# Optimization experiments

Measured on AMD Instinct MI355X. Metric: run time of the kernel, lower is better.

The kernel has to match this reference:

```python
import jax, jax.numpy as jnp
import numpy as np

B, N, D = 4, 4096, 1024
LN_EPS = 1e-5

def setup_inputs() -> dict:
    key = jax.random.key(0)
    ks = jax.random.split(key, 12)
    s = 1.0 / np.sqrt(D)
    return {
        "embeddings": jax.random.normal(ks[0], (B, N, D), dtype=jnp.float32),
        "edge_indices": jax.random.randint(ks[1], (2, 8192), 0, N, dtype=jnp.int64),
        "edge_times": jax.random.uniform(ks[2], (8192,), dtype=jnp.float32),
        "timestamps": jax.random.uniform(ks[3], (N,), dtype=jnp.float32),
        "Wq": jax.random.uniform(ks[4], (D, D), jnp.float32, -s, s),
        "bq": jax.random.uniform(ks[5], (D,), jnp.float32, -s, s),
        "Wk": jax.random.uniform(ks[6], (D, D), jnp.float32, -s, s),
        "bk": jax.random.uniform(ks[7], (D,), jnp.float32, -s, s),
        "Wv": jax.random.uniform(ks[8], (D, D), jnp.float32, -s, s),
        "bv": jax.random.uniform(ks[9], (D,), jnp.float32, -s, s),
        "gamma": jnp.ones((D,), jnp.float32),
        "beta": jnp.zeros((D,), jnp.float32),
    }

def reference(embeddings, edge_indices, edge_times, timestamps,
              Wq, bq, Wk, bk, Wv, bv, gamma, beta):
    # edge_indices / edge_times / timestamps are unused by the original forward.
    d = embeddings.shape[-1]
    q = jnp.einsum("bnd,ed->bne", embeddings, Wq) + bq   # [B,N,D]
    k = jnp.einsum("bnd,ed->bne", embeddings, Wk) + bk
    v = jnp.einsum("bnd,ed->bne", embeddings, Wv) + bv
    scores = jnp.einsum("bnd,bmd->bnm", q, k) / jnp.sqrt(jnp.asarray(d, embeddings.dtype))
    attn = jax.nn.softmax(scores, axis=-1)                # [B,N,N]
    attended = jnp.einsum("bnm,bmd->bnd", attn, v)
    x = embeddings + attended
    mu = jnp.mean(x, axis=-1, keepdims=True)
    var = jnp.mean(jnp.square(x - mu), axis=-1, keepdims=True)
    return gamma * (x - mu) * jax.lax.rsqrt(var + LN_EPS) + beta
```

## Files before the change

kernel.cpp:

```cpp
#include <hip/hip_runtime.h>
#include <hip/hip_fp8.h>

typedef unsigned short u16;
typedef unsigned char  u8;
typedef long long      i64;
using bf16x8 = __attribute__((ext_vector_type(8))) __bf16;
using f32x4  = __attribute__((ext_vector_type(4))) float;
using i64x2  = __attribute__((ext_vector_type(2))) long long;

__device__ __forceinline__ u16 f2bf(float f) {
    unsigned u = __builtin_bit_cast(unsigned, f);
    u += 0x7fffu + ((u >> 16) & 1u);
    return (u16)(u >> 16);
}
__device__ __forceinline__ float bf2f(u16 h) {
    unsigned u = ((unsigned)h) << 16;
    return __builtin_bit_cast(float, u);
}
__device__ __forceinline__ u8 f2fp8(float f) {
    __hip_fp8_e4m3 t(f);
    return t.__x;
}
__device__ __forceinline__ float wred_sum(float v) {
    #pragma unroll
    for (int o = 32; o; o >>= 1) v += __shfl_xor(v, o, 64);
    return v;
}

__device__ __forceinline__ void gl2lds16(const void* g, void* l) {
    __builtin_amdgcn_global_load_lds(
        (__attribute__((address_space(1))) void*)(g),
        (__attribute__((address_space(3))) void*)(l), 16, 0, 0);
}

#define SBAR0() __builtin_amdgcn_sched_barrier(0)

__global__ __launch_bounds__(256)
void cast_bf16(const float* __restrict__ src, u16* __restrict__ dst, int n4) {
    int i = blockIdx.x * 256 + threadIdx.x;
    if (i < n4) {
        float4 f = ((const float4*)src)[i];
        ushort4 u;
        u.x = f2bf(f.x); u.y = f2bf(f.y); u.z = f2bf(f.z); u.w = f2bf(f.w);
        ((ushort4*)dst)[i] = u;
    }
}

template<int MODE>
__global__ __launch_bounds__(512, 2)
void gemm256(const u16* __restrict__ A, const u16* __restrict__ Bt,
             u16* __restrict__ oQ, u16* __restrict__ oK,
             const float* __restrict__ bQ, const float* __restrict__ bK,
             const float* __restrict__ bV,
             u8* __restrict__ oP, u8* __restrict__ oP2,
             float* __restrict__ sums, const float scale)
{
    __shared__ u16 smem[65536];
    const int tid = threadIdx.x;
    const int wv = tid >> 6, lane = tid & 63;
    const int wm = wv >> 2, wn = wv & 3;
    const int row0 = blockIdx.x << 8, col0 = blockIdx.y << 8;

    const size_t boff = (size_t)blockIdx.z * 4194304;
    const int srow = tid >> 2;
    const int scol = ((tid & 3) ^ ((tid >> 3) & 3)) << 3;
    const u16* gA = A + boff + (size_t)(row0 + srow) * 1024 + scol;
    const u16* gB = Bt + boff + (size_t)(col0 + srow) * 1024 + scol;
    char* lds = (char*)smem;
    const int wvo = wv << 10;

    const int fr = lane & 15, g = lane >> 4;
    const int kc = (g ^ ((fr >> 1) & 3)) << 4;

    f32x4 acc[8][4];
    #pragma unroll
    for (int i = 0; i < 8; i++)
        #pragma unroll
        for (int j = 0; j < 4; j++) acc[i][j] = (f32x4){0.f, 0.f, 0.f, 0.f};

    #define SG_A(ts, sl) { \
        gl2lds16(gA + (ts) * 32,          lds + (sl) * 32768 + wvo); \
        gl2lds16(gA + 131072 + (ts) * 32, lds + (sl) * 32768 + 8192 + wvo); }
    #define SG_B(ts, sl) { \
        gl2lds16(gB + (ts) * 32,          lds + (sl) * 32768 + 16384 + wvo); \
        gl2lds16(gB + 131072 + (ts) * 32, lds + (sl) * 32768 + 24576 + wvo); }

    SG_A(0, 0); SG_B(0, 0);
    SG_A(1, 1); SG_B(1, 1);
    SG_A(2, 2); SG_B(2, 2);
    asm volatile("s_waitcnt vmcnt(8)" ::: "memory");
    __builtin_amdgcn_s_barrier();
    SBAR0();

    for (int t = 0; t < 32; ++t) {
        const int slot = t & 3;
        const int ts = (t + 3) & 31;
        const int ns = (t + 3) & 3;
        const char* Ab = lds + slot * 32768;
        const char* Bb = Ab + 16384;

        SG_A(ts, ns);
        bf16x8 bf[4], af[4];
        #pragma unroll
        for (int j = 0; j < 4; ++j)
            bf[j] = *(const bf16x8*)(Bb + (wn * 64 + 16 * j + fr) * 64 + kc);
        #pragma unroll
        for (int i = 0; i < 4; ++i)
            af[i] = *(const bf16x8*)(Ab + (wm * 128 + 16 * i + fr) * 64 + kc);
        SBAR0();
        __builtin_amdgcn_s_barrier();
        asm volatile("s_waitcnt lgkmcnt(0)" ::: "memory");
        SBAR0();
        __builtin_amdgcn_s_setprio(1);
        #pragma unroll
        for (int i = 0; i < 4; ++i)
            #pragma unroll
            for (int j = 0; j < 4; ++j)
                acc[i][j] = __builtin_amdgcn_mfma_f32_16x16x32_bf16(af[i], bf[j], acc[i][j], 0, 0, 0);
        __builtin_amdgcn_s_setprio(0);

        SG_B(ts, ns);
        bf16x8 af2[4];
        #pragma unroll
        for (int i = 0; i < 4; ++i)
            af2[i] = *(const bf16x8*)(Ab + (wm * 128 + 64 + 16 * i + fr) * 64 + kc);
        asm volatile("s_waitcnt vmcnt(8) lgkmcnt(0)" ::: "memory");
        SBAR0();
        __builtin_amdgcn_s_barrier();
        SBAR0();
        __builtin_amdgcn_s_setprio(1);
        #pragma unroll
        for (int i = 0; i < 4; ++i)
            #pragma unroll
            for (int j = 0; j < 4; ++j)
                acc[i + 4][j] = __builtin_amdgcn_mfma_f32_16x16x32_bf16(af2[i], bf[j], acc[i + 4][j], 0, 0, 0);
        __builtin_amdgcn_s_setprio(0);
    }
    #undef SG_A
    #undef SG_B

    asm volatile("s_waitcnt vmcnt(0)" ::: "memory");

    const int rB = (lane >> 4) << 2, cB = lane & 15;

    if (MODE == 0) {
        const int sel = col0 >> 10;
        if (sel < 2) {
            const float* bias = (sel == 0) ? bQ : bK;
            u16* dst = (sel == 0) ? oQ : oK;
            #pragma unroll
            for (int i = 0; i < 8; i++) {
                #pragma unroll
                for (int j = 0; j < 4; j++) {
                    const int m0 = row0 + wm * 128 + 16 * i + rB;
                    const int e  = (col0 & 1023) + wn * 64 + 16 * j + cB;
                    const float bb = bias[e];
                    #pragma unroll
                    for (int t = 0; t < 4; t++)
                        dst[(size_t)(m0 + t) * 1024 + e] = f2bf(acc[i][j][t] + bb);
                }
            }
        } else {
            const int b      = row0 >> 12;
            const int n_base = row0 & 4095;
            const int e0     = col0 & 1023;
            unsigned* lds32 = (unsigned*)smem;
            __syncthreads();
            #pragma unroll
            for (int i = 0; i < 8; i++) {
                const int n_l0 = wm * 128 + 16 * i + rB;
                const int blk  = n_l0 >> 6;
                const int q    = (n_l0 & 63) >> 2;
                const int pd   = ((q >> 1) & 3) * 4 + ((q >> 3) << 1) + (q & 1);
                const int dwi  = blk * 16 + pd;
                const int G    = dwi >> 2;
                const int kq   = dwi & 3;
                #pragma unroll
                for (int j = 0; j < 4; j++) {
                    const int e_p = wn * 64 + 16 * j + cB;
                    const float bb = bV[e0 + e_p];
                    union { u8 c[4]; unsigned u; } pk;
                    pk.c[0] = f2fp8(acc[i][j][0] + bb);
                    pk.c[1] = f2fp8(acc[i][j][1] + bb);
                    pk.c[2] = f2fp8(acc[i][j][2] + bb);
                    pk.c[3] = f2fp8(acc[i][j][3] + bb);
                    lds32[e_p * 64 + ((G ^ (e_p & 15)) << 2) + kq] = pk.u;
                }
            }
            __syncthreads();
            #pragma unroll
            for (int it = 0; it < 8; ++it) {
                const int idx = it * 512 + tid;
                const int er  = idx >> 4;
                const int c16 = idx & 15;
                int4 v = *(const int4*)&lds32[er * 64 + ((c16 ^ (er & 15)) << 2)];
                *(int4*)&oP[(size_t)b * 4194304 +
                            (size_t)(e0 + er) * 4096 + n_base + c16 * 16] = v;
            }
        }
    } else {
        u8* Pz = blockIdx.z ? oP2 : oP;
        float* smz = sums + (blockIdx.z << 12);
        float psum[8][4];
        #pragma unroll
        for (int i = 0; i < 8; i++)
            #pragma unroll
            for (int t = 0; t < 4; t++) psum[i][t] = 0.f;

        #pragma unroll
        for (int i = 0; i < 8; i++) {
            const int m0 = row0 + wm * 128 + 16 * i + rB;
            #pragma unroll
            for (int j = 0; j < 4; j++) {
                const int n64 = 16 * j + cB;
                const int p   = ((n64 >> 3) & 3) * 16 + ((n64 >> 5) << 3) + (cB & 7);
                const int c   = col0 + wn * 64 + p;
                #pragma unroll
                for (int t = 0; t < 4; t++) {
                    const float e = __expf(acc[i][j][t] * scale);
                    psum[i][t] += e;
                    Pz[(size_t)(m0 + t) * 4096 + c] = f2fp8(e);
                }
            }
        }
        #pragma unroll
        for (int i = 0; i < 8; i++) {
            #pragma unroll
            for (int t = 0; t < 4; t++) {
                float v = psum[i][t];
                v += __shfl_xor(v, 1, 64);
                v += __shfl_xor(v, 2, 64);
                v += __shfl_xor(v, 4, 64);
                v += __shfl_xor(v, 8, 64);
                if (cB == 0)
                    atomicAdd(&smz[row0 + wm * 128 + 16 * i + rB + t], v);
            }
        }
    }
}

__global__ __launch_bounds__(512, 2)
void pv256(const u8* __restrict__ p0, const u8* __restrict__ p1,
           const u8* __restrict__ p2, const u8* __restrict__ p3,
           const u8* __restrict__ vt8, const float* __restrict__ sums,
           float* __restrict__ out)
{
    __shared__ u8 smem[131072];
    const int b = blockIdx.z;
    const u8* Pb = (b == 0) ? p0 : (b == 1) ? p1 : (b == 2) ? p2 : p3;
    const u8* Vb = vt8 + (size_t)b * 4194304;
    const float* sm = sums + (b << 12);
    float* Ob = out + (size_t)b * 4194304;

    const int tid = threadIdx.x;
    const int wv = tid >> 6, lane = tid & 63;
    const int wm = wv >> 2, wn = wv & 3;
    const int row0 = blockIdx.x << 8, col0 = blockIdx.y << 8;

    const int srow = tid >> 2;
    const int sc16 = ((tid & 3) ^ ((tid >> 3) & 3)) << 4;
    const u8* gA = Pb + (size_t)(row0 + srow) * 4096 + sc16;
    const u8* gB = Vb + (size_t)(col0 + srow) * 4096 + sc16;
    char* lds = (char*)smem;
    const int wvo = wv << 10;

    const int fr = lane & 15, g = lane >> 4;
    const int pc = ((g ^ ((fr >> 1) & 3)) << 4);

    f32x4 acc[8][4];
    #pragma unroll
    for (int i = 0; i < 8; i++)
        #pragma unroll
        for (int j = 0; j < 4; j++) acc[i][j] = (f32x4){0.f, 0.f, 0.f, 0.f};

    #define PG_A(ts, sl) { \
        gl2lds16(gA + (ts) * 64,          lds + (sl) * 32768 + wvo); \
        gl2lds16(gA + 524288 + (ts) * 64, lds + (sl) * 32768 + 8192 + wvo); }
    #define PG_B(ts, sl) { \
        gl2lds16(gB + (ts) * 64,          lds + (sl) * 32768 + 16384 + wvo); \
        gl2lds16(gB + 524288 + (ts) * 64, lds + (sl) * 32768 + 24576 + wvo); }

    PG_A(0, 0); PG_B(0, 0);
    PG_A(1, 1); PG_B(1, 1);
    PG_A(2, 2); PG_B(2, 2);
    asm volatile("s_waitcnt vmcnt(8)" ::: "memory");
    __builtin_amdgcn_s_barrier();
    SBAR0();

    for (int t = 0; t < 64; ++t) {
        const int slot = t & 3;
        const int ts = (t + 3) & 63;
        const int ns = (t + 3) & 3;
        const char* Ab = lds + slot * 32768;
        const char* Bb = Ab + 16384;

        PG_A(ts, ns);
        i64x2 av[8], bv[4];
        #pragma unroll
        for (int j = 0; j < 4; ++j)
            bv[j] = *(const i64x2*)(Bb + (wn * 64 + 16 * j + fr) * 64 + pc);
        #pragma unroll
        for (int i = 0; i < 8; ++i)
            av[i] = *(const i64x2*)(Ab + (wm * 128 + 16 * i + fr) * 64 + pc);
        SBAR0();
        __builtin_amdgcn_s_barrier();
        asm volatile("s_waitcnt lgkmcnt(0)" ::: "memory");
        SBAR0();
        __builtin_amdgcn_s_setprio(1);
        #pragma unroll
        for (int i = 0; i < 8; ++i)
            #pragma unroll
            for (int j = 0; j < 4; ++j)
                acc[i][j] = __builtin_amdgcn_mfma_f32_16x16x32_fp8_fp8(av[i][0], bv[j][0], acc[i][j], 0, 0, 0);
        __builtin_amdgcn_s_setprio(0);

        PG_B(ts, ns);
        asm volatile("s_waitcnt vmcnt(8)" ::: "memory");
        SBAR0();
        __builtin_amdgcn_s_barrier();
        SBAR0();
        __builtin_amdgcn_s_setprio(1);
        #pragma unroll
        for (int i = 0; i < 8; ++i)
            #pragma unroll
            for (int j = 0; j < 4; ++j)
                acc[i][j] = __builtin_amdgcn_mfma_f32_16x16x32_fp8_fp8(av[i][1], bv[j][1], acc[i][j], 0, 0, 0);
        __builtin_amdgcn_s_setprio(0);
    }
    #undef PG_A
    #undef PG_B

    asm volatile("s_waitcnt vmcnt(0)" ::: "memory");

    const int rB = (lane >> 4) << 2, cB = lane & 15;
    #pragma unroll
    for (int i = 0; i < 8; i++) {
        const int m0 = row0 + wm * 128 + 16 * i + rB;
        const float i0 = 1.0f / sm[m0];
        const float i1 = 1.0f / sm[m0 + 1];
        const float i2 = 1.0f / sm[m0 + 2];
        const float i3 = 1.0f / sm[m0 + 3];
        #pragma unroll
        for (int j = 0; j < 4; j++) {
            const int e = col0 + wn * 64 + 16 * j + cB;
            Ob[(size_t)(m0 + 0) * 1024 + e] = acc[i][j][0] * i0;
            Ob[(size_t)(m0 + 1) * 1024 + e] = acc[i][j][1] * i1;
            Ob[(size_t)(m0 + 2) * 1024 + e] = acc[i][j][2] * i2;
            Ob[(size_t)(m0 + 3) * 1024 + e] = acc[i][j][3] * i3;
        }
    }
}

__global__ __launch_bounds__(256)
void residual_ln(const float* __restrict__ emb, float* __restrict__ out,
                 const float* __restrict__ gamma, const float* __restrict__ beta) {
    const size_t row = blockIdx.x;
    const int t = threadIdx.x;
    const int wv = t >> 6, lane = t & 63;
    const size_t base = row * 1024 + t * 4;

    float4 ev = *(const float4*)(emb + base);
    float4 ov = *(const float4*)(out + base);
    float x0 = ev.x + ov.x, x1 = ev.y + ov.y, x2 = ev.z + ov.z, x3 = ev.w + ov.w;

    float s = x0 + x1 + x2 + x3;
    float q = x0 * x0 + x1 * x1 + x2 * x2 + x3 * x3;
    s = wred_sum(s);
    q = wred_sum(q);
    __shared__ float s1[4], s2[4];
    if (lane == 0) { s1[wv] = s; s2[wv] = q; }
    __syncthreads();
    s = s1[0] + s1[1] + s1[2] + s1[3];
    q = s2[0] + s2[1] + s2[2] + s2[3];

    const float mu  = s * (1.0f / 1024.0f);
    const float var = q * (1.0f / 1024.0f) - mu * mu;
    const float r   = rsqrtf(var + 1e-5f);

    float4 g  = *(const float4*)(gamma + t * 4);
    float4 be = *(const float4*)(beta + t * 4);
    float4 res;
    res.x = (x0 - mu) * r * g.x + be.x;
    res.y = (x1 - mu) * r * g.y + be.y;
    res.z = (x2 - mu) * r * g.z + be.z;
    res.w = (x3 - mu) * r * g.w + be.w;
    *(float4*)(out + base) = res;
}

extern "C" void kernel_launch(void* const* d_in, const int* in_sizes, int n_in,
                              void* d_out, int out_size, void* d_ws, size_t ws_size,
                              hipStream_t stream) {
    const float* emb   = (const float*)d_in[0];
    const float* Wq    = (const float*)d_in[4];
    const float* bq    = (const float*)d_in[5];
    const float* Wk    = (const float*)d_in[6];
    const float* bk    = (const float*)d_in[7];
    const float* Wv    = (const float*)d_in[8];
    const float* bv    = (const float*)d_in[9];
    const float* gamma = (const float*)d_in[10];
    const float* beta  = (const float*)d_in[11];
    float* out = (float*)d_out;

    char* ws = (char*)d_ws;
    if (ws_size < 140509184u) return;
    u16* Xbf = (u16*)(ws);
    u16* Wbf = (u16*)(ws + 33554432);
    u16* Qbf = (u16*)(ws + 39845888);
    u16* Kbf = (u16*)(ws + 73400320);

    u8*    P0   = (u8*)(ws);
    u8*    P1   = (u8*)(ws + 16777216);
    float* SUMS = (float*)(ws + 33554432);
    u8*    P3   = (u8*)(ws + 39845888);
    u8*    VT8  = (u8*)(ws + 106954752);
    u8*    P2   = (u8*)(ws + 123731968);

    cast_bf16<<<16384, 256, 0, stream>>>(emb, Xbf, 4194304);
    cast_bf16<<<1024, 256, 0, stream>>>(Wq, Wbf,           262144);
    cast_bf16<<<1024, 256, 0, stream>>>(Wk, Wbf + 1048576, 262144);
    cast_bf16<<<1024, 256, 0, stream>>>(Wv, Wbf + 2097152, 262144);

    gemm256<0><<<dim3(64, 12), 512, 0, stream>>>(Xbf, Wbf,
        Qbf, Kbf, bq, bk, bv, VT8, nullptr, nullptr, 1.0f);

    hipMemsetAsync(SUMS, 0, 65536, stream);

    gemm256<1><<<dim3(16, 16, 2), 512, 0, stream>>>(Qbf, Kbf,
        nullptr, nullptr, nullptr, nullptr, nullptr,
        P0, P1, SUMS, 0.03125f);
    gemm256<1><<<dim3(16, 16, 2), 512, 0, stream>>>(Qbf + 2 * 4194304, Kbf + 2 * 4194304,
        nullptr, nullptr, nullptr, nullptr, nullptr,
        P2, P3, SUMS + 8192, 0.03125f);

    pv256<<<dim3(16, 4, 4), 512, 0, stream>>>(P0, P1, P2, P3, VT8, SUMS, out);

    residual_ln<<<16384, 256, 0, stream>>>(emb, out, gamma, beta);
}
```

Before: 547.7 us.

## Merge cast kernels, fold log2e into scale, relax waitcnt before barrier

Replaces four separate fp32-to-bf16 cast launches with one kernel that picks its source and destination from the block index, which removes launch overhead. The softmax exponent now uses the hardware exp2 intrinsic, with log2(e) folded into the scale passed from the host. In the GEMM main loop, the LDS wait (lgkmcnt) now comes after the barrier instead of before it, which may let LDS reads overlap the barrier. The exp2 builtin may lose some accuracy compared with __expf, which probably matters little because the result is rounded to fp8 anyway.

Measured after the change: 540.5 us. About the same (-1.3%).

```diff
diff --git a/kernel.cpp b/kernel.cpp
--- a/kernel.cpp
+++ b/kernel.cpp
@@ -36,14 +36,26 @@
 #define SBAR0() __builtin_amdgcn_sched_barrier(0)
 
 __global__ __launch_bounds__(256)
-void cast_bf16(const float* __restrict__ src, u16* __restrict__ dst, int n4) {
-    int i = blockIdx.x * 256 + threadIdx.x;
-    if (i < n4) {
-        float4 f = ((const float4*)src)[i];
-        ushort4 u;
-        u.x = f2bf(f.x); u.y = f2bf(f.y); u.z = f2bf(f.z); u.w = f2bf(f.w);
-        ((ushort4*)dst)[i] = u;
+void cast_all(const float* __restrict__ emb,
+              const float* __restrict__ wq, const float* __restrict__ wk,
+              const float* __restrict__ wv,
+              u16* __restrict__ xbf, u16* __restrict__ wbf) {
+    const int b = blockIdx.x;
+    const float* src;
+    u16* dst;
+    int blk;
+    if (b < 16384) { src = emb; dst = xbf; blk = b; }
+    else {
+        const int s = (b - 16384) >> 10;
+        src = (s == 0) ? wq : (s == 1) ? wk : wv;
+        dst = wbf + s * 1048576;
+        blk = (b - 16384) & 1023;
     }
+    const int i = blk * 256 + threadIdx.x;
+    float4 f = ((const float4*)src)[i];
+    ushort4 u;
+    u.x = f2bf(f.x); u.y = f2bf(f.y); u.z = f2bf(f.z); u.w = f2bf(f.w);
+    ((ushort4*)dst)[i] = u;
 }
 
 template<int MODE>
@@ -124,9 +136,10 @@
         #pragma unroll
         for (int i = 0; i < 4; ++i)
             af2[i] = *(const bf16x8*)(Ab + (wm * 128 + 64 + 16 * i + fr) * 64 + kc);
-        asm volatile("s_waitcnt vmcnt(8) lgkmcnt(0)" ::: "memory");
+        asm volatile("s_waitcnt vmcnt(8)" ::: "memory");
         SBAR0();
         __builtin_amdgcn_s_barrier();
+        asm volatile("s_waitcnt lgkmcnt(0)" ::: "memory");
         SBAR0();
         __builtin_amdgcn_s_setprio(1);
         #pragma unroll
@@ -217,7 +230,7 @@
                 const int c   = col0 + wn * 64 + p;
                 #pragma unroll
                 for (int t = 0; t < 4; t++) {
-                    const float e = __expf(acc[i][j][t] * scale);
+                    const float e = __builtin_amdgcn_exp2f(acc[i][j][t] * scale);
                     psum[i][t] += e;
                     Pz[(size_t)(m0 + t) * 4096 + c] = f2fp8(e);
                 }
@@ -415,22 +428,20 @@
     u8*    VT8  = (u8*)(ws + 106954752);
     u8*    P2   = (u8*)(ws + 123731968);
 
-    cast_bf16<<<16384, 256, 0, stream>>>(emb, Xbf, 4194304);
-    cast_bf16<<<1024, 256, 0, stream>>>(Wq, Wbf,           262144);
-    cast_bf16<<<1024, 256, 0, stream>>>(Wk, Wbf + 1048576, 262144);
-    cast_bf16<<<1024, 256, 0, stream>>>(Wv, Wbf + 2097152, 262144);
+    cast_all<<<19456, 256, 0, stream>>>(emb, Wq, Wk, Wv, Xbf, Wbf);
 
     gemm256<0><<<dim3(64, 12), 512, 0, stream>>>(Xbf, Wbf,
         Qbf, Kbf, bq, bk, bv, VT8, nullptr, nullptr, 1.0f);
 
     hipMemsetAsync(SUMS, 0, 65536, stream);
 
+    const float lscale = 0.03125f * 1.4426950408889634f;
     gemm256<1><<<dim3(16, 16, 2), 512, 0, stream>>>(Qbf, Kbf,
         nullptr, nullptr, nullptr, nullptr, nullptr,
-        P0, P1, SUMS, 0.03125f);
+        P0, P1, SUMS, lscale);
     gemm256<1><<<dim3(16, 16, 2), 512, 0, stream>>>(Qbf + 2 * 4194304, Kbf + 2 * 4194304,
         nullptr, nullptr, nullptr, nullptr, nullptr,
-        P2, P3, SUMS + 8192, 0.03125f);
+        P2, P3, SUMS + 8192, lscale);
 
     pv256<<<dim3(16, 4, 4), 512, 0, stream>>>(P0, P1, P2, P3, VT8, SUMS, out);
 
```
